# Kernel optimization log

Measured on AMD Instinct MI355X. Metric: run time of the kernel, lower is better.

The kernel has to match this reference:

```python
import jax, jax.numpy as jnp
import numpy as np
from functools import partial


def _lstm_cell(x, h, c, W_ih, W_hh, b_ih, b_hh):
    # PyTorch gate layout along the 4H dim: i, f, g, o
    gates = x @ W_ih.T + h @ W_hh.T + (b_ih + b_hh)  # [B, 4H]
    i, f, g, o = jnp.split(gates, 4, axis=-1)
    i = jax.nn.sigmoid(i)
    f = jax.nn.sigmoid(f)
    g = jnp.tanh(g)
    o = jax.nn.sigmoid(o)
    c_new = f * c + i * g
    h_new = o * jnp.tanh(c_new)
    return h_new, c_new


def setup_inputs() -> dict:
    key = jax.random.key(0)
    ks = jax.random.split(key, 5)
    B, S, H = 2048, 64, 256
    scale = 1.0 / np.sqrt(H)
    return {
        "x_0": jax.random.normal(ks[0], (B, S, H), dtype=jnp.float32),
        "W_ih": jax.random.uniform(ks[1], (4 * H, H), jnp.float32, -scale, scale),
        "W_hh": jax.random.uniform(ks[2], (4 * H, H), jnp.float32, -scale, scale),
        "b_ih": jax.random.uniform(ks[3], (4 * H,), jnp.float32, -scale, scale),
        "b_hh": jax.random.uniform(ks[4], (4 * H,), jnp.float32, -scale, scale),
        "n_steps": 32,
    }


def reference(x_0, W_ih, W_hh, b_ih, b_hh, n_steps):
    B = x_0.shape[0]
    H = W_hh.shape[1]
    h0 = jnp.zeros((B, H), dtype=x_0.dtype)
    c0 = jnp.zeros((B, H), dtype=x_0.dtype)

    cell = partial(_lstm_cell, W_ih=W_ih, W_hh=W_hh, b_ih=b_ih, b_hh=b_hh)

    # Encode the input sequence.
    def enc_step(carry, x_t):
        h, c = carry
        h, c = cell(x_t, h, c)
        return (h, c), None

    (h, c), _ = jax.lax.scan(enc_step, (h0, c0), x_0.swapaxes(0, 1))  # scan over S

    def ar_step(carry, _):
        hh, cc = carry
        hh, cc = cell(hh, hh, cc)
        return (hh, cc), hh

    _, preds = jax.lax.scan(ar_step, (h, c), None, length=n_steps)  # [n_steps, B, H]

    prediction = jnp.concatenate([h[:, None, :], preds.swapaxes(0, 1)], axis=1)
    return prediction  # [B, n_steps+1, H]
```

## Files before the change

### kernel.cpp

```cpp
#include <hip/hip_runtime.h>
#include <cstdint>
#include <cstddef>

#define B_    2048
#define H_    256
#define S_    64
#define NSTEP 32
#define OUTS  33
#define N4H   1024
#define XROWSTRIDE (S_ * H_)
#define EPI_STRIDE 260
#define NBLK  256
#define CNT_STRIDE 16

typedef _Float16 f16;
typedef _Float16 f16x4 __attribute__((ext_vector_type(4)));
typedef _Float16 f16x8 __attribute__((ext_vector_type(8)));
typedef float    f32x4 __attribute__((ext_vector_type(4)));

__device__ __forceinline__ float sigm(float x)  { return 1.f / (1.f + __expf(-x)); }
__device__ __forceinline__ float tanh_(float x) { return 1.f - 2.f / (1.f + __expf(2.f * x)); }

__device__ __forceinline__ int sa_off(int t16, int slot) {
    return (t16 * 64 + (slot ^ (t16 & 7))) * 8;
}

#define PIN8(A) asm volatile("" : "+v"((A)[0]), "+v"((A)[1]), "+v"((A)[2]), "+v"((A)[3]), \
                                  "+v"((A)[4]), "+v"((A)[5]), "+v"((A)[6]), "+v"((A)[7]))

__device__ __forceinline__ f16x4 ld_h8(const f16* p) {
    unsigned long long v = __hip_atomic_load((const unsigned long long*)p,
                                             __ATOMIC_RELAXED, __HIP_MEMORY_SCOPE_SYSTEM);
    return __builtin_bit_cast(f16x4, v);
}
__device__ __forceinline__ void st_h2(f16* p, f16 v) {
    __hip_atomic_store((unsigned short*)p, __builtin_bit_cast(unsigned short, v),
                       __ATOMIC_RELAXED, __HIP_MEMORY_SCOPE_SYSTEM);
}

__device__ __forceinline__ void gsync(unsigned* cnt, unsigned target) {
    asm volatile("s_waitcnt vmcnt(0)" ::: "memory");
    __syncthreads();
    if (threadIdx.x == 0) {
        __hip_atomic_fetch_add(cnt, 1u, __ATOMIC_RELAXED, __HIP_MEMORY_SCOPE_SYSTEM);
        unsigned spins = 0;
        while (__hip_atomic_load(cnt, __ATOMIC_RELAXED, __HIP_MEMORY_SCOPE_SYSTEM) < target) {
            __builtin_amdgcn_s_sleep(1);
            if (++spins > (1u << 20)) break;
        }
    }
    __syncthreads();
    asm volatile("" ::: "memory");
}

__global__ __launch_bounds__(256) void prep_kernel(
    const float* __restrict__ W_ih, const float* __restrict__ W_hh,
    const float* __restrict__ b_ih, const float* __restrict__ b_hh,
    f16* __restrict__ WeP, f16* __restrict__ WaP, float* __restrict__ pb)
{
    int t = blockIdx.x * 256 + threadIdx.x;
    if (t < N4H * 64) {
        int n  = t >> 6;
        int kc = (t & 63) * 8;
        int j = n >> 2, g = n & 3;
        const float* src = (kc < H_) ? &W_ih[(size_t)(g * H_ + j) * H_ + kc]
                                     : &W_hh[(size_t)(g * H_ + j) * H_ + kc - H_];
        f16x8 v;
#pragma unroll
        for (int e = 0; e < 8; ++e) v[e] = (f16)src[e];
        int ct = n >> 4, c15 = n & 15, kk = kc >> 5, q = (kc >> 3) & 3;
        *(f16x8*)&WeP[((size_t)(ct * 16 + kk) * 64 + q * 16 + c15) * 8] = v;
    } else if (t < N4H * 64 + N4H * 32) {
        int u  = t - N4H * 64;
        int n  = u >> 5;
        int kc = (u & 31) * 8;
        int j = n >> 2, g = n & 3;
        const float* s1 = &W_ih[(size_t)(g * H_ + j) * H_ + kc];
        const float* s2 = &W_hh[(size_t)(g * H_ + j) * H_ + kc];
        f16x8 v;
#pragma unroll
        for (int e = 0; e < 8; ++e) v[e] = (f16)(s1[e] + s2[e]);
        int ct = n >> 4, c15 = n & 15, kk = kc >> 5, q = (kc >> 3) & 3;
        *(f16x8*)&WaP[((size_t)(ct * 8 + kk) * 64 + q * 16 + c15) * 8] = v;
    } else if (t < N4H * 64 + N4H * 32 + N4H) {
        int n = t - (N4H * 64 + N4H * 32);
        int j = n >> 2, g = n & 3;
        pb[n] = b_ih[g * H_ + j] + b_hh[g * H_ + j];
    }
}

__global__ __attribute__((amdgpu_waves_per_eu(1, 1))) __launch_bounds__(256)
void lstm_fused(
    const float* __restrict__ x0,
    const f16*  __restrict__ WeP,
    const f16*  __restrict__ WaP,
    const float* __restrict__ pb,
    f16* __restrict__ hb0, f16* __restrict__ hb1,
    unsigned* __restrict__ cnts,
    float* __restrict__ out)
{
    __shared__ __align__(16) unsigned char smem[32 * EPI_STRIDE * 4];
    f16*   sA   = (f16*)smem;
    float* sEpi = (float*)smem;

    const int tid = threadIdx.x;
    const int l   = tid & 63;
    const int w   = tid >> 6;
    const int bid = blockIdx.x;
    const int n   = (bid >> 3) & 3;
    const int m   = (bid & 7) + ((bid >> 5) << 3);
    const int b0  = m * 32;
    unsigned* cnt = &cnts[m * CNT_STRIDE];
    unsigned phase = 0;

    const int srow = tid >> 3;
    const int kseg = (tid & 7) * 32;
    const int smt  = srow >> 4, slrow = srow & 15;

    f16* hbuf[2] = {hb0, hb1};

    f16x8 Bf[4][16];
#pragma unroll
    for (int f = 0; f < 4; ++f) {
        const int ct = n * 16 + w * 4 + f;
#pragma unroll
        for (int kk = 0; kk < 16; ++kk)
            Bf[f][kk] = *(const f16x8*)&WeP[((size_t)(ct * 16 + kk) * 64 + l) * 8];
    }
#pragma unroll
    for (int f = 0; f < 4; ++f) { PIN8(&Bf[f][0]); PIN8(&Bf[f][8]); }

    const f32x4 pbr = *(const f32x4*)&pb[n * 256 + l * 4];

    float cs[8];
#pragma unroll
    for (int i = 0; i < 8; ++i) cs[i] = 0.f;

    const int q = l >> 4, c15 = l & 15;

    float4 xv[8];
    {
        const float* src = x0 + (size_t)(b0 + srow) * XROWSTRIDE + kseg;
#pragma unroll
        for (int qq = 0; qq < 8; ++qq) xv[qq] = *(const float4*)(src + qq * 4);
    }

    for (int t = 0; t < S_; ++t) {
        {
            const int kkA = kseg >> 5;
#pragma unroll
            for (int qq = 0; qq < 4; ++qq) {
                float4 v0 = xv[qq * 2], v1 = xv[qq * 2 + 1];
                f16x8 h8;
                h8[0]=(f16)v0.x; h8[1]=(f16)v0.y; h8[2]=(f16)v0.z; h8[3]=(f16)v0.w;
                h8[4]=(f16)v1.x; h8[5]=(f16)v1.y; h8[6]=(f16)v1.z; h8[7]=(f16)v1.w;
                *(f16x8*)&sA[sa_off(smt * 16 + kkA, qq * 16 + slrow)] = h8;
            }
            const f16* hsrc = hbuf[t & 1] + (size_t)(b0 + srow) * H_ + kseg;
            const int kkH = 8 + (kseg >> 5);
#pragma unroll
            for (int qq = 0; qq < 4; ++qq) {
                f16x4 lo = ld_h8(hsrc + qq * 8);
                f16x4 hi = ld_h8(hsrc + qq * 8 + 4);
                f16x8 h8;
#pragma unroll
                for (int e = 0; e < 4; ++e) { h8[e] = lo[e]; h8[4 + e] = hi[e]; }
                *(f16x8*)&sA[sa_off(smt * 16 + kkH, qq * 16 + slrow)] = h8;
            }
        }
        __syncthreads();

        f32x4 acc[2][4];
#pragma unroll
        for (int mt = 0; mt < 2; ++mt)
#pragma unroll
            for (int f = 0; f < 4; ++f) acc[mt][f] = (f32x4){0.f, 0.f, 0.f, 0.f};
#pragma unroll
        for (int kk = 0; kk < 16; ++kk) {
            f16x8 a0 = *(const f16x8*)&sA[sa_off(kk, l)];
            f16x8 a1 = *(const f16x8*)&sA[sa_off(16 + kk, l)];
#pragma unroll
            for (int f = 0; f < 4; ++f) {
                acc[0][f] = __builtin_amdgcn_mfma_f32_16x16x32_f16(a0, Bf[f][kk], acc[0][f], 0, 0, 0);
                acc[1][f] = __builtin_amdgcn_mfma_f32_16x16x32_f16(a1, Bf[f][kk], acc[1][f], 0, 0, 0);
            }
        }
        __syncthreads();

        if (t + 1 < S_) {
            const float* src = x0 + (size_t)(b0 + srow) * XROWSTRIDE + (t + 1) * H_ + kseg;
#pragma unroll
            for (int qq = 0; qq < 8; ++qq) xv[qq] = *(const float4*)(src + qq * 4);
        }

#pragma unroll
        for (int mt = 0; mt < 2; ++mt)
#pragma unroll
            for (int f = 0; f < 4; ++f)
#pragma unroll
                for (int r = 0; r < 4; ++r)
                    sEpi[(mt * 16 + q * 4 + r) * EPI_STRIDE + w * 64 + f * 16 + c15] = acc[mt][f][r];
        __syncthreads();

        f16* hdst = hbuf[(t + 1) & 1];
#pragma unroll
        for (int i = 0; i < 8; ++i) {
            const int row = i * 4 + w;
            f32x4 g4 = *(const f32x4*)&sEpi[row * EPI_STRIDE + l * 4];
            float vi = g4[0] + pbr[0];
            float vf = g4[1] + pbr[1];
            float vg = g4[2] + pbr[2];
            float vo = g4[3] + pbr[3];
            float ig = sigm(vi), fg = sigm(vf), gg = tanh_(vg), og = sigm(vo);
            float cn = fg * cs[i] + ig * gg;
            float hn = og * tanh_(cn);
            cs[i] = cn;
            st_h2(&hdst[(size_t)(b0 + row) * H_ + n * 64 + l], (f16)hn);
            if (t == S_ - 1)
                out[(size_t)(b0 + row) * (OUTS * H_) + n * 64 + l] = hn;
        }
        gsync(cnt, (++phase) * 4u);
    }

#pragma unroll
    for (int f = 0; f < 4; ++f) {
        const int ct = n * 16 + w * 4 + f;
#pragma unroll
        for (int kk = 0; kk < 8; ++kk)
            Bf[f][kk] = *(const f16x8*)&WaP[((size_t)(ct * 8 + kk) * 64 + l) * 8];
    }
#pragma unroll
    for (int f = 0; f < 4; ++f) PIN8(&Bf[f][0]);

    for (int t = 0; t < NSTEP; ++t) {
        {
            const f16* hsrc = hbuf[t & 1] + (size_t)(b0 + srow) * H_ + kseg;
            const int kkH = kseg >> 5;
#pragma unroll
            for (int qq = 0; qq < 4; ++qq) {
                f16x4 lo = ld_h8(hsrc + qq * 8);
                f16x4 hi = ld_h8(hsrc + qq * 8 + 4);
                f16x8 h8;
#pragma unroll
                for (int e = 0; e < 4; ++e) { h8[e] = lo[e]; h8[4 + e] = hi[e]; }
                *(f16x8*)&sA[sa_off(smt * 8 + kkH, qq * 16 + slrow)] = h8;
            }
        }
        __syncthreads();

        f32x4 acc[2][4];
#pragma unroll
        for (int mt = 0; mt < 2; ++mt)
#pragma unroll
            for (int f = 0; f < 4; ++f) acc[mt][f] = (f32x4){0.f, 0.f, 0.f, 0.f};
#pragma unroll
        for (int kk = 0; kk < 8; ++kk) {
            f16x8 a0 = *(const f16x8*)&sA[sa_off(kk, l)];
            f16x8 a1 = *(const f16x8*)&sA[sa_off(8 + kk, l)];
#pragma unroll
            for (int f = 0; f < 4; ++f) {
                acc[0][f] = __builtin_amdgcn_mfma_f32_16x16x32_f16(a0, Bf[f][kk], acc[0][f], 0, 0, 0);
                acc[1][f] = __builtin_amdgcn_mfma_f32_16x16x32_f16(a1, Bf[f][kk], acc[1][f], 0, 0, 0);
            }
        }
        __syncthreads();

#pragma unroll
        for (int mt = 0; mt < 2; ++mt)
#pragma unroll
            for (int f = 0; f < 4; ++f)
#pragma unroll
                for (int r = 0; r < 4; ++r)
                    sEpi[(mt * 16 + q * 4 + r) * EPI_STRIDE + w * 64 + f * 16 + c15] = acc[mt][f][r];
        __syncthreads();

        f16* hdst = hbuf[(t + 1) & 1];
#pragma unroll
        for (int i = 0; i < 8; ++i) {
            const int row = i * 4 + w;
            f32x4 g4 = *(const f32x4*)&sEpi[row * EPI_STRIDE + l * 4];
            float vi = g4[0] + pbr[0];
            float vf = g4[1] + pbr[1];
            float vg = g4[2] + pbr[2];
            float vo = g4[3] + pbr[3];
            float ig = sigm(vi), fg = sigm(vf), gg = tanh_(vg), og = sigm(vo);
            float cn = fg * cs[i] + ig * gg;
            float hn = og * tanh_(cn);
            cs[i] = cn;
            st_h2(&hdst[(size_t)(b0 + row) * H_ + n * 64 + l], (f16)hn);
            out[(size_t)(b0 + row) * (OUTS * H_) + (size_t)(t + 1) * H_ + n * 64 + l] = hn;
        }
        if (t + 1 < NSTEP) gsync(cnt, (++phase) * 4u);
    }
}

extern "C" void kernel_launch(void* const* d_in, const int* in_sizes, int n_in,
                              void* d_out, int out_size, void* d_ws, size_t ws_size,
                              hipStream_t stream) {
    const float* x0   = (const float*)d_in[0];
    const float* W_ih = (const float*)d_in[1];
    const float* W_hh = (const float*)d_in[2];
    const float* b_ih = (const float*)d_in[3];
    const float* b_hh = (const float*)d_in[4];
    float* out = (float*)d_out;

    char* p = (char*)d_ws;
    f16* WeP = (f16*)p; p += (size_t)N4H * 512 * 2;
    f16* WaP = (f16*)p; p += (size_t)N4H * 256 * 2;
    float* pb = (float*)p; p += (size_t)N4H * 4;
    f16* hb0 = (f16*)p; p += (size_t)B_ * H_ * 2;
    f16* hb1 = (f16*)p; p += (size_t)B_ * H_ * 2;
    unsigned* cnts = (unsigned*)p; p += (size_t)64 * CNT_STRIDE * 4;

    hipMemsetAsync(hb0, 0, (size_t)B_ * H_ * 2, stream);
    hipMemsetAsync(cnts, 0, (size_t)64 * CNT_STRIDE * 4, stream);

    const int prep_total = N4H * 64 + N4H * 32 + N4H;
    prep_kernel<<<dim3((prep_total + 255) / 256), dim3(256), 0, stream>>>(
        W_ih, W_hh, b_ih, b_hh, WeP, WaP, pb);

    lstm_fused<<<dim3(NBLK), dim3(256), 0, stream>>>(
        x0, WeP, WaP, pb, hb0, hb1, cnts, out);
}
```

Measured before the change: 707.0 us.

## Split-K across 8 waves and overlap next x-projection with grid barrier wait

Doubles the block to 512 threads, with two wave groups each taking half of the K dimension and reducing through a two-slot epilogue buffer. This halves the register-resident weights per wave. The barrier is split into arrive and wait, and the next step's input projection x@W_ih is computed between them so the latency of the cross-block sync is hidden by work that does not depend on h. It also vectorizes the h stores to 64-bit and changes the LDS swizzle and padding, at the cost of more LDS traffic and an extra reduction add.

```diff
diff --git a/kernel.cpp b/kernel.cpp
--- a/kernel.cpp
+++ b/kernel.cpp
@@ -9,7 +9,7 @@
 #define OUTS  33
 #define N4H   1024
 #define XROWSTRIDE (S_ * H_)
-#define EPI_STRIDE 260
+#define EPI_STRIDE 268
 #define NBLK  256
 #define CNT_STRIDE 16
 
@@ -17,40 +17,31 @@
 typedef _Float16 f16x4 __attribute__((ext_vector_type(4)));
 typedef _Float16 f16x8 __attribute__((ext_vector_type(8)));
 typedef float    f32x4 __attribute__((ext_vector_type(4)));
+typedef unsigned long long u64;
 
 __device__ __forceinline__ float sigm(float x)  { return 1.f / (1.f + __expf(-x)); }
 __device__ __forceinline__ float tanh_(float x) { return 1.f - 2.f / (1.f + __expf(2.f * x)); }
 
-__device__ __forceinline__ int sa_off(int t16, int slot) {
-    return (t16 * 64 + (slot ^ (t16 & 7))) * 8;
+__device__ __forceinline__ int sa2(int t16, int slot) {
+    return (t16 * 64 + (slot ^ ((t16 & 7) << 2))) * 8;
 }
 
 #define PIN8(A) asm volatile("" : "+v"((A)[0]), "+v"((A)[1]), "+v"((A)[2]), "+v"((A)[3]), \
                                   "+v"((A)[4]), "+v"((A)[5]), "+v"((A)[6]), "+v"((A)[7]))
-
-__device__ __forceinline__ f16x4 ld_h8(const f16* p) {
-    unsigned long long v = __hip_atomic_load((const unsigned long long*)p,
-                                             __ATOMIC_RELAXED, __HIP_MEMORY_SCOPE_SYSTEM);
-    return __builtin_bit_cast(f16x4, v);
-}
-__device__ __forceinline__ void st_h2(f16* p, f16 v) {
-    __hip_atomic_store((unsigned short*)p, __builtin_bit_cast(unsigned short, v),
-                       __ATOMIC_RELAXED, __HIP_MEMORY_SCOPE_SYSTEM);
-}
-
-__device__ __forceinline__ void gsync(unsigned* cnt, unsigned target) {
-    asm volatile("s_waitcnt vmcnt(0)" ::: "memory");
-    __syncthreads();
-    if (threadIdx.x == 0) {
-        __hip_atomic_fetch_add(cnt, 1u, __ATOMIC_RELAXED, __HIP_MEMORY_SCOPE_SYSTEM);
-        unsigned spins = 0;
-        while (__hip_atomic_load(cnt, __ATOMIC_RELAXED, __HIP_MEMORY_SCOPE_SYSTEM) < target) {
-            __builtin_amdgcn_s_sleep(1);
-            if (++spins > (1u << 20)) break;
-        }
-    }
-    __syncthreads();
-    asm volatile("" ::: "memory");
+#define PIN4(A) asm volatile("" : "+v"((A)[0]), "+v"((A)[1]), "+v"((A)[2]), "+v"((A)[3]))
+
+__device__ __forceinline__ u64 ld64sys(const f16* p) {
+    return __hip_atomic_load((const u64*)p, __ATOMIC_RELAXED, __HIP_MEMORY_SCOPE_SYSTEM);
+}
+__device__ __forceinline__ void st64sys(f16* p, u64 v) {
+    __hip_atomic_store((u64*)p, v, __ATOMIC_RELAXED, __HIP_MEMORY_SCOPE_SYSTEM);
+}
+__device__ __forceinline__ f16x8 pack8(u64 a, u64 b) {
+    f16x4 x = __builtin_bit_cast(f16x4, a), y = __builtin_bit_cast(f16x4, b);
+    f16x8 r;
+    r[0] = x[0]; r[1] = x[1]; r[2] = x[2]; r[3] = x[3];
+    r[4] = y[0]; r[5] = y[1]; r[6] = y[2]; r[7] = y[3];
+    return r;
 }
 
 __global__ __launch_bounds__(256) void prep_kernel(
@@ -89,7 +80,7 @@
     }
 }
 
-__global__ __attribute__((amdgpu_waves_per_eu(1, 1))) __launch_bounds__(256)
+__global__ __attribute__((amdgpu_waves_per_eu(2, 2))) __launch_bounds__(512)
 void lstm_fused(
     const float* __restrict__ x0,
     const f16*  __restrict__ WeP,
@@ -99,171 +90,220 @@
     unsigned* __restrict__ cnts,
     float* __restrict__ out)
 {
-    __shared__ __align__(16) unsigned char smem[32 * EPI_STRIDE * 4];
-    f16*   sA   = (f16*)smem;
-    float* sEpi = (float*)smem;
-
-    const int tid = threadIdx.x;
-    const int l   = tid & 63;
-    const int w   = tid >> 6;
-    const int bid = blockIdx.x;
-    const int n   = (bid >> 3) & 3;
-    const int m   = (bid & 7) + ((bid >> 5) << 3);
-    const int b0  = m * 32;
-    unsigned* cnt = &cnts[m * CNT_STRIDE];
+    __shared__ __align__(16) f16   sAx[16 * 64 * 8];
+    __shared__ __align__(16) f16   sAh[16 * 64 * 8];
+    __shared__ __align__(16) float sEpi[2][32][EPI_STRIDE];
+
+    const int tid  = threadIdx.x;
+    const int l    = tid & 63;
+    const int w    = tid >> 6;
+    const int wp   = w & 3;
+    const int half = w >> 2;
+    const int bid  = blockIdx.x;
+    const int n    = (bid >> 3) & 3;
+    const int m    = (bid & 7) + ((bid >> 5) << 3);
+    const int b0   = m * 32;
+    unsigned* cnt  = &cnts[m * CNT_STRIDE];
     unsigned phase = 0;
 
-    const int srow = tid >> 3;
-    const int kseg = (tid & 7) * 32;
-    const int smt  = srow >> 4, slrow = srow & 15;
+    const int srow  = tid >> 4;
+    const int chunk = tid & 15;
+    const int s_c15 = srow & 15, s_mt = srow >> 4;
+    const int s_kk  = chunk >> 1, s_q2 = chunk & 1;
+    const int crow = tid >> 4;
+    const int jl4  = (tid & 15) * 4;
+    const int q4 = (l >> 4) * 4, c15 = l & 15;
 
     f16* hbuf[2] = {hb0, hb1};
 
-    f16x8 Bf[4][16];
+    f16x8 Bf[4][8];
 #pragma unroll
     for (int f = 0; f < 4; ++f) {
-        const int ct = n * 16 + w * 4 + f;
-#pragma unroll
-        for (int kk = 0; kk < 16; ++kk)
-            Bf[f][kk] = *(const f16x8*)&WeP[((size_t)(ct * 16 + kk) * 64 + l) * 8];
-    }
-#pragma unroll
-    for (int f = 0; f < 4; ++f) { PIN8(&Bf[f][0]); PIN8(&Bf[f][8]); }
-
-    const f32x4 pbr = *(const f32x4*)&pb[n * 256 + l * 4];
-
-    float cs[8];
-#pragma unroll
-    for (int i = 0; i < 8; ++i) cs[i] = 0.f;
-
-    const int q = l >> 4, c15 = l & 15;
-
-    float4 xv[8];
+        const int ct = n * 16 + wp * 4 + f;
+#pragma unroll
+        for (int jj = 0; jj < 8; ++jj) {
+            const int kk = 2 * jj + half;
+            Bf[f][jj] = *(const f16x8*)&WeP[((size_t)(ct * 16 + kk) * 64 + l) * 8];
+        }
+    }
+#pragma unroll
+    for (int f = 0; f < 4; ++f) PIN8(&Bf[f][0]);
+
+    float cs[4] = {0.f, 0.f, 0.f, 0.f};
+
+    f32x4 acc[2][4];
+
     {
-        const float* src = x0 + (size_t)(b0 + srow) * XROWSTRIDE + kseg;
-#pragma unroll
-        for (int qq = 0; qq < 8; ++qq) xv[qq] = *(const float4*)(src + qq * 4);
+        const float* xs = x0 + (size_t)(b0 + srow) * XROWSTRIDE + chunk * 16;
+        float4 v0 = *(const float4*)(xs + 0), v1 = *(const float4*)(xs + 4);
+        float4 v2 = *(const float4*)(xs + 8), v3 = *(const float4*)(xs + 12);
+        f16x8 lo, hi;
+        lo[0]=(f16)v0.x; lo[1]=(f16)v0.y; lo[2]=(f16)v0.z; lo[3]=(f16)v0.w;
+        lo[4]=(f16)v1.x; lo[5]=(f16)v1.y; lo[6]=(f16)v1.z; lo[7]=(f16)v1.w;
+        hi[0]=(f16)v2.x; hi[1]=(f16)v2.y; hi[2]=(f16)v2.z; hi[3]=(f16)v2.w;
+        hi[4]=(f16)v3.x; hi[5]=(f16)v3.y; hi[6]=(f16)v3.z; hi[7]=(f16)v3.w;
+        *(f16x8*)&sAx[sa2(s_mt * 8 + s_kk, (s_q2 * 2 + 0) * 16 + s_c15)] = lo;
+        *(f16x8*)&sAx[sa2(s_mt * 8 + s_kk, (s_q2 * 2 + 1) * 16 + s_c15)] = hi;
+    }
+    __syncthreads();
+#pragma unroll
+    for (int mt = 0; mt < 2; ++mt)
+#pragma unroll
+        for (int f = 0; f < 4; ++f) acc[mt][f] = (f32x4){0.f, 0.f, 0.f, 0.f};
+#pragma unroll
+    for (int jj = 0; jj < 4; ++jj) {
+        const int kk = 2 * jj + half;
+        f16x8 a0 = *(const f16x8*)&sAx[sa2(0 * 8 + kk, l)];
+        f16x8 a1 = *(const f16x8*)&sAx[sa2(1 * 8 + kk, l)];
+#pragma unroll
+        for (int f = 0; f < 4; ++f) {
+            acc[0][f] = __builtin_amdgcn_mfma_f32_16x16x32_f16(a0, Bf[f][jj], acc[0][f], 0, 0, 0);
+            acc[1][f] = __builtin_amdgcn_mfma_f32_16x16x32_f16(a1, Bf[f][jj], acc[1][f], 0, 0, 0);
+        }
     }
 
     for (int t = 0; t < S_; ++t) {
         {
-            const int kkA = kseg >> 5;
-#pragma unroll
-            for (int qq = 0; qq < 4; ++qq) {
-                float4 v0 = xv[qq * 2], v1 = xv[qq * 2 + 1];
-                f16x8 h8;
-                h8[0]=(f16)v0.x; h8[1]=(f16)v0.y; h8[2]=(f16)v0.z; h8[3]=(f16)v0.w;
-                h8[4]=(f16)v1.x; h8[5]=(f16)v1.y; h8[6]=(f16)v1.z; h8[7]=(f16)v1.w;
-                *(f16x8*)&sA[sa_off(smt * 16 + kkA, qq * 16 + slrow)] = h8;
-            }
-            const f16* hsrc = hbuf[t & 1] + (size_t)(b0 + srow) * H_ + kseg;
-            const int kkH = 8 + (kseg >> 5);
-#pragma unroll
-            for (int qq = 0; qq < 4; ++qq) {
-                f16x4 lo = ld_h8(hsrc + qq * 8);
-                f16x4 hi = ld_h8(hsrc + qq * 8 + 4);
-                f16x8 h8;
-#pragma unroll
-                for (int e = 0; e < 4; ++e) { h8[e] = lo[e]; h8[4 + e] = hi[e]; }
-                *(f16x8*)&sA[sa_off(smt * 16 + kkH, qq * 16 + slrow)] = h8;
-            }
-        }
-        __syncthreads();
-
-        f32x4 acc[2][4];
+            const f16* hsrc = hbuf[t & 1] + (size_t)(b0 + srow) * H_ + chunk * 16;
+            u64 d0 = ld64sys(hsrc + 0), d1 = ld64sys(hsrc + 4);
+            u64 d2 = ld64sys(hsrc + 8), d3 = ld64sys(hsrc + 12);
+            *(f16x8*)&sAh[sa2(s_mt * 8 + s_kk, (s_q2 * 2 + 0) * 16 + s_c15)] = pack8(d0, d1);
+            *(f16x8*)&sAh[sa2(s_mt * 8 + s_kk, (s_q2 * 2 + 1) * 16 + s_c15)] = pack8(d2, d3);
+        }
+        __syncthreads();
+
+#pragma unroll
+        for (int jj = 0; jj < 4; ++jj) {
+            const int kkh = 2 * jj + half;
+            f16x8 a0 = *(const f16x8*)&sAh[sa2(0 * 8 + kkh, l)];
+            f16x8 a1 = *(const f16x8*)&sAh[sa2(1 * 8 + kkh, l)];
+#pragma unroll
+            for (int f = 0; f < 4; ++f) {
+                acc[0][f] = __builtin_amdgcn_mfma_f32_16x16x32_f16(a0, Bf[f][4 + jj], acc[0][f], 0, 0, 0);
+                acc[1][f] = __builtin_amdgcn_mfma_f32_16x16x32_f16(a1, Bf[f][4 + jj], acc[1][f], 0, 0, 0);
+            }
+        }
+
 #pragma unroll
         for (int mt = 0; mt < 2; ++mt)
 #pragma unroll
-            for (int f = 0; f < 4; ++f) acc[mt][f] = (f32x4){0.f, 0.f, 0.f, 0.f};
-#pragma unroll
-        for (int kk = 0; kk < 16; ++kk) {
-            f16x8 a0 = *(const f16x8*)&sA[sa_off(kk, l)];
-            f16x8 a1 = *(const f16x8*)&sA[sa_off(16 + kk, l)];
-#pragma unroll
-            for (int f = 0; f < 4; ++f) {
-                acc[0][f] = __builtin_amdgcn_mfma_f32_16x16x32_f16(a0, Bf[f][kk], acc[0][f], 0, 0, 0);
-                acc[1][f] = __builtin_amdgcn_mfma_f32_16x16x32_f16(a1, Bf[f][kk], acc[1][f], 0, 0, 0);
-            }
-        }
-        __syncthreads();
+            for (int f = 0; f < 4; ++f)
+#pragma unroll
+                for (int r = 0; r < 4; ++r)
+                    sEpi[half][mt * 16 + q4 + r][wp * 64 + f * 16 + c15] = acc[mt][f][r];
+        __syncthreads();
+
+        {
+            f16* hdst = hbuf[(t + 1) & 1];
+            const float* pbb = pb + n * 256 + jl4 * 4;
+            float hvv[4];
+            f16x4 hf;
+#pragma unroll
+            for (int jj = 0; jj < 4; ++jj) {
+                f32x4 ga = *(const f32x4*)&sEpi[0][crow][(jl4 + jj) * 4];
+                f32x4 gb = *(const f32x4*)&sEpi[1][crow][(jl4 + jj) * 4];
+                f32x4 pv = *(const f32x4*)&pbb[jj * 4];
+                float vi = ga[0] + gb[0] + pv[0];
+                float vf = ga[1] + gb[1] + pv[1];
+                float vg = ga[2] + gb[2] + pv[2];
+                float vo = ga[3] + gb[3] + pv[3];
+                float ig = sigm(vi), fg = sigm(vf), gg = tanh_(vg), og = sigm(vo);
+                float cn = fg * cs[jj] + ig * gg;
+                float hn = og * tanh_(cn);
+                cs[jj] = cn; hvv[jj] = hn; hf[jj] = (f16)hn;
+            }
+            st64sys(&hdst[(size_t)(b0 + crow) * H_ + n * 64 + jl4],
+                    __builtin_bit_cast(u64, hf));
+            if (t == S_ - 1) {
+                float4 o = {hvv[0], hvv[1], hvv[2], hvv[3]};
+                *(float4*)&out[(size_t)(b0 + crow) * (OUTS * H_) + n * 64 + jl4] = o;
+            }
+        }
+
+        ++phase;
+        asm volatile("s_waitcnt vmcnt(0)" ::: "memory");
+        __syncthreads();
+        if (tid == 0)
+            __hip_atomic_fetch_add(cnt, 1u, __ATOMIC_RELAXED, __HIP_MEMORY_SCOPE_SYSTEM);
 
         if (t + 1 < S_) {
-            const float* src = x0 + (size_t)(b0 + srow) * XROWSTRIDE + (t + 1) * H_ + kseg;
-#pragma unroll
-            for (int qq = 0; qq < 8; ++qq) xv[qq] = *(const float4*)(src + qq * 4);
-        }
-
-#pragma unroll
-        for (int mt = 0; mt < 2; ++mt)
-#pragma unroll
-            for (int f = 0; f < 4; ++f)
-#pragma unroll
-                for (int r = 0; r < 4; ++r)
-                    sEpi[(mt * 16 + q * 4 + r) * EPI_STRIDE + w * 64 + f * 16 + c15] = acc[mt][f][r];
-        __syncthreads();
-
-        f16* hdst = hbuf[(t + 1) & 1];
-#pragma unroll
-        for (int i = 0; i < 8; ++i) {
-            const int row = i * 4 + w;
-            f32x4 g4 = *(const f32x4*)&sEpi[row * EPI_STRIDE + l * 4];
-            float vi = g4[0] + pbr[0];
-            float vf = g4[1] + pbr[1];
-            float vg = g4[2] + pbr[2];
-            float vo = g4[3] + pbr[3];
-            float ig = sigm(vi), fg = sigm(vf), gg = tanh_(vg), og = sigm(vo);
-            float cn = fg * cs[i] + ig * gg;
-            float hn = og * tanh_(cn);
-            cs[i] = cn;
-            st_h2(&hdst[(size_t)(b0 + row) * H_ + n * 64 + l], (f16)hn);
-            if (t == S_ - 1)
-                out[(size_t)(b0 + row) * (OUTS * H_) + n * 64 + l] = hn;
-        }
-        gsync(cnt, (++phase) * 4u);
+            {
+                const float* xs = x0 + (size_t)(b0 + srow) * XROWSTRIDE + (t + 1) * H_ + chunk * 16;
+                float4 v0 = *(const float4*)(xs + 0), v1 = *(const float4*)(xs + 4);
+                float4 v2 = *(const float4*)(xs + 8), v3 = *(const float4*)(xs + 12);
+                f16x8 lo, hi;
+                lo[0]=(f16)v0.x; lo[1]=(f16)v0.y; lo[2]=(f16)v0.z; lo[3]=(f16)v0.w;
+                lo[4]=(f16)v1.x; lo[5]=(f16)v1.y; lo[6]=(f16)v1.z; lo[7]=(f16)v1.w;
+                hi[0]=(f16)v2.x; hi[1]=(f16)v2.y; hi[2]=(f16)v2.z; hi[3]=(f16)v2.w;
+                hi[4]=(f16)v3.x; hi[5]=(f16)v3.y; hi[6]=(f16)v3.z; hi[7]=(f16)v3.w;
+                *(f16x8*)&sAx[sa2(s_mt * 8 + s_kk, (s_q2 * 2 + 0) * 16 + s_c15)] = lo;
+                *(f16x8*)&sAx[sa2(s_mt * 8 + s_kk, (s_q2 * 2 + 1) * 16 + s_c15)] = hi;
+            }
+            __syncthreads();
+#pragma unroll
+            for (int mt = 0; mt < 2; ++mt)
+#pragma unroll
+                for (int f = 0; f < 4; ++f) acc[mt][f] = (f32x4){0.f, 0.f, 0.f, 0.f};
+#pragma unroll
+            for (int jj = 0; jj < 4; ++jj) {
+                const int kk = 2 * jj + half;
+                f16x8 a0 = *(const f16x8*)&sAx[sa2(0 * 8 + kk, l)];
+                f16x8 a1 = *(const f16x8*)&sAx[sa2(1 * 8 + kk, l)];
+#pragma unroll
+                for (int f = 0; f < 4; ++f) {
+                    acc[0][f] = __builtin_amdgcn_mfma_f32_16x16x32_f16(a0, Bf[f][jj], acc[0][f], 0, 0, 0);
+                    acc[1][f] = __builtin_amdgcn_mfma_f32_16x16x32_f16(a1, Bf[f][jj], acc[1][f], 0, 0, 0);
+                }
+            }
+        }
+
+        if (tid == 0) {
+            unsigned spins = 0;
+            while (__hip_atomic_load(cnt, __ATOMIC_RELAXED, __HIP_MEMORY_SCOPE_SYSTEM) < phase * 4u) {
+                __builtin_amdgcn_s_sleep(1);
+                if (++spins > (1u << 20)) break;
+            }
+        }
+        __syncthreads();
     }
 
 #pragma unroll
     for (int f = 0; f < 4; ++f) {
-        const int ct = n * 16 + w * 4 + f;
-#pragma unroll
-        for (int kk = 0; kk < 8; ++kk)
-            Bf[f][kk] = *(const f16x8*)&WaP[((size_t)(ct * 8 + kk) * 64 + l) * 8];
-    }
-#pragma unroll
-    for (int f = 0; f < 4; ++f) PIN8(&Bf[f][0]);
+        const int ct = n * 16 + wp * 4 + f;
+#pragma unroll
+        for (int jj = 0; jj < 4; ++jj) {
+            const int kk = 2 * jj + half;
+            Bf[f][jj] = *(const f16x8*)&WaP[((size_t)(ct * 8 + kk) * 64 + l) * 8];
+        }
+    }
+#pragma unroll
+    for (int f = 0; f < 4; ++f) PIN4(&Bf[f][0]);
 
     for (int t = 0; t < NSTEP; ++t) {
         {
-            const f16* hsrc = hbuf[t & 1] + (size_t)(b0 + srow) * H_ + kseg;
-            const int kkH = kseg >> 5;
-#pragma unroll
-            for (int qq = 0; qq < 4; ++qq) {
-                f16x4 lo = ld_h8(hsrc + qq * 8);
-                f16x4 hi = ld_h8(hsrc + qq * 8 + 4);
-                f16x8 h8;
-#pragma unroll
-                for (int e = 0; e < 4; ++e) { h8[e] = lo[e]; h8[4 + e] = hi[e]; }
-                *(f16x8*)&sA[sa_off(smt * 8 + kkH, qq * 16 + slrow)] = h8;
-            }
-        }
-        __syncthreads();
-
-        f32x4 acc[2][4];
+            const f16* hsrc = hbuf[t & 1] + (size_t)(b0 + srow) * H_ + chunk * 16;
+            u64 d0 = ld64sys(hsrc + 0), d1 = ld64sys(hsrc + 4);
+            u64 d2 = ld64sys(hsrc + 8), d3 = ld64sys(hsrc + 12);
+            *(f16x8*)&sAh[sa2(s_mt * 8 + s_kk, (s_q2 * 2 + 0) * 16 + s_c15)] = pack8(d0, d1);
+            *(f16x8*)&sAh[sa2(s_mt * 8 + s_kk, (s_q2 * 2 + 1) * 16 + s_c15)] = pack8(d2, d3);
+        }
+        __syncthreads();
+
 #pragma unroll
         for (int mt = 0; mt < 2; ++mt)
 #pragma unroll
             for (int f = 0; f < 4; ++f) acc[mt][f] = (f32x4){0.f, 0.f, 0.f, 0.f};
 #pragma unroll
-        for (int kk = 0; kk < 8; ++kk) {
-            f16x8 a0 = *(const f16x8*)&sA[sa_off(kk, l)];
-            f16x8 a1 = *(const f16x8*)&sA[sa_off(8 + kk, l)];
+        for (int jj = 0; jj < 4; ++jj) {
+            const int kk = 2 * jj + half;
+            f16x8 a0 = *(const f16x8*)&sAh[sa2(0 * 8 + kk, l)];
+            f16x8 a1 = *(const f16x8*)&sAh[sa2(1 * 8 + kk, l)];
 #pragma unroll
             for (int f = 0; f < 4; ++f) {
-                acc[0][f] = __builtin_amdgcn_mfma_f32_16x16x32_f16(a0, Bf[f][kk], acc[0][f], 0, 0, 0);
-                acc[1][f] = __builtin_amdgcn_mfma_f32_16x16x32_f16(a1, Bf[f][kk], acc[1][f], 0, 0, 0);
-            }
-        }
-        __syncthreads();
+                acc[0][f] = __builtin_amdgcn_mfma_f32_16x16x32_f16(a0, Bf[f][jj], acc[0][f], 0, 0, 0);
+                acc[1][f] = __builtin_amdgcn_mfma_f32_16x16x32_f16(a1, Bf[f][jj], acc[1][f], 0, 0, 0);
+            }
+        }
 
 #pragma unroll
         for (int mt = 0; mt < 2; ++mt)
@@ -271,26 +311,48 @@
             for (int f = 0; f < 4; ++f)
 #pragma unroll
                 for (int r = 0; r < 4; ++r)
-                    sEpi[(mt * 16 + q * 4 + r) * EPI_STRIDE + w * 64 + f * 16 + c15] = acc[mt][f][r];
-        __syncthreads();
-
-        f16* hdst = hbuf[(t + 1) & 1];
-#pragma unroll
-        for (int i = 0; i < 8; ++i) {
-            const int row = i * 4 + w;
-            f32x4 g4 = *(const f32x4*)&sEpi[row * EPI_STRIDE + l * 4];
-            float vi = g4[0] + pbr[0];
-            float vf = g4[1] + pbr[1];
-            float vg = g4[2] + pbr[2];
-            float vo = g4[3] + pbr[3];
-            float ig = sigm(vi), fg = sigm(vf), gg = tanh_(vg), og = sigm(vo);
-            float cn = fg * cs[i] + ig * gg;
-            float hn = og * tanh_(cn);
-            cs[i] = cn;
-            st_h2(&hdst[(size_t)(b0 + row) * H_ + n * 64 + l], (f16)hn);
-            out[(size_t)(b0 + row) * (OUTS * H_) + (size_t)(t + 1) * H_ + n * 64 + l] = hn;
-        }
-        if (t + 1 < NSTEP) gsync(cnt, (++phase) * 4u);
+                    sEpi[half][mt * 16 + q4 + r][wp * 64 + f * 16 + c15] = acc[mt][f][r];
+        __syncthreads();
+
+        {
+            f16* hdst = hbuf[(t + 1) & 1];
+            const float* pbb = pb + n * 256 + jl4 * 4;
+            float hvv[4];
+            f16x4 hf;
+#pragma unroll
+            for (int jj = 0; jj < 4; ++jj) {
+                f32x4 ga = *(const f32x4*)&sEpi[0][crow][(jl4 + jj) * 4];
+                f32x4 gb = *(const f32x4*)&sEpi[1][crow][(jl4 + jj) * 4];
+                f32x4 pv = *(const f32x4*)&pbb[jj * 4];
+                float vi = ga[0] + gb[0] + pv[0];
+                float vf = ga[1] + gb[1] + pv[1];
+                float vg = ga[2] + gb[2] + pv[2];
+                float vo = ga[3] + gb[3] + pv[3];
+                float ig = sigm(vi), fg = sigm(vf), gg = tanh_(vg), og = sigm(vo);
+                float cn = fg * cs[jj] + ig * gg;
+                float hn = og * tanh_(cn);
+                cs[jj] = cn; hvv[jj] = hn; hf[jj] = (f16)hn;
+            }
+            st64sys(&hdst[(size_t)(b0 + crow) * H_ + n * 64 + jl4],
+                    __builtin_bit_cast(u64, hf));
+            float4 o = {hvv[0], hvv[1], hvv[2], hvv[3]};
+            *(float4*)&out[(size_t)(b0 + crow) * (OUTS * H_) + (size_t)(t + 1) * H_ + n * 64 + jl4] = o;
+        }
+
+        if (t + 1 < NSTEP) {
+            ++phase;
+            asm volatile("s_waitcnt vmcnt(0)" ::: "memory");
+            __syncthreads();
+            if (tid == 0) {
+                __hip_atomic_fetch_add(cnt, 1u, __ATOMIC_RELAXED, __HIP_MEMORY_SCOPE_SYSTEM);
+                unsigned spins = 0;
+                while (__hip_atomic_load(cnt, __ATOMIC_RELAXED, __HIP_MEMORY_SCOPE_SYSTEM) < phase * 4u) {
+                    __builtin_amdgcn_s_sleep(1);
+                    if (++spins > (1u << 20)) break;
+                }
+            }
+            __syncthreads();
+        }
     }
 }
 
@@ -319,6 +381,6 @@
     prep_kernel<<<dim3((prep_total + 255) / 256), dim3(256), 0, stream>>>(
         W_ih, W_hh, b_ih, b_hh, WeP, WaP, pb);
 
-    lstm_fused<<<dim3(NBLK), dim3(256), 0, stream>>>(
+    lstm_fused<<<dim3(NBLK), dim3(512), 0, stream>>>(
         x0, WeP, WaP, pb, hb0, hb1, cnts, out);
 }
```

Result: faster. 612.7 us (-13.3%).
